# Performance work log

Measured on AMD Instinct MI355X. Metric: run time of the kernel, lower is better.

The kernel has to match this reference:

```python
import jax, jax.numpy as jnp
import numpy as np

NUM_HEADS = 16


def setup_inputs() -> dict:
    key = jax.random.key(0)
    k1, k2, k3 = jax.random.split(key, 3)
    x = jax.random.normal(k1, (2, 2048, 1024), dtype=jnp.float32)
    w_qkv = jax.random.normal(k2, (3072, 1024), dtype=jnp.float32) * 0.02
    b_qkv = jax.random.normal(k3, (3072,), dtype=jnp.float32) * 0.02
    return {"x": x, "w_qkv": w_qkv, "b_qkv": b_qkv}


def reference(x, w_qkv, b_qkv):
    b, s, _ = x.shape
    d_model = w_qkv.shape[0] // 3
    head_dim = d_model // NUM_HEADS
    # fused QKV projection (torch Linear: x @ W^T + b)
    qkv = x @ w_qkv.T + b_qkv                      # [b, s, 3*d_model]
    qkv = qkv.reshape(b, s, NUM_HEADS, 3 * head_dim)
    qkv = jnp.transpose(qkv, (0, 2, 1, 3))          # [b, h, s, 3*hd]
    q, k, v = jnp.split(qkv, 3, axis=-1)            # each [b, h, s, hd]
    scale = 1.0 / np.sqrt(head_dim).astype(np.float32)
    scores = jnp.einsum("bhqd,bhkd->bhqk", q, k) * scale
    attn = jax.nn.softmax(scores, axis=-1)
    values = jnp.einsum("bhqk,bhkd->bhqd", attn, v)  # [b, h, s, hd]
    # Faithful to source: reshape WITHOUT permuting heads back (head-interleaved)
    return values.reshape(b, s, d_model)
```

## Files before the change

kernel.cpp:

```cpp
#include <hip/hip_runtime.h>
#include <cstdint>

typedef unsigned short ushort_t;

#define M_ROWS 4096
#define N_COLS 3072
#define K_DIM  1024
#define S_LEN  2048
#define NHEADS 16
#define HDIM   64
#define QSCALE 0.1803368801111204f

typedef __bf16 bf16_t;
typedef bf16_t  bf16x8  __attribute__((ext_vector_type(8)));
typedef short   shortx4 __attribute__((ext_vector_type(4)));
typedef float   floatx4 __attribute__((ext_vector_type(4)));
typedef ushort_t ushortx4 __attribute__((ext_vector_type(4)));

union U32x2S4 { unsigned u[2]; shortx4 s; };

__device__ __forceinline__ unsigned short f2bf(float f) {
  unsigned u = __float_as_uint(f);
  u += 0x7FFFu + ((u >> 16) & 1u);
  return (unsigned short)(u >> 16);
}

__device__ __forceinline__ unsigned pkbf(float a, float b) {
  unsigned ua = __float_as_uint(a) + 0x8000u;
  unsigned ub = __float_as_uint(b) + 0x8000u;
  return __builtin_amdgcn_perm(ub, ua, 0x07060302u);
}

__device__ __forceinline__ unsigned cvtpk(float a, float b) {
#if __has_builtin(__builtin_amdgcn_cvt_pk_bf16_f32)
  auto t = __builtin_amdgcn_cvt_pk_bf16_f32(a, b);
  unsigned r;
  __builtin_memcpy(&r, &t, 4);
  return r;
#else
  return pkbf(a, b);
#endif
}

__device__ __forceinline__ float fexp2(float x) {
#if __has_builtin(__builtin_amdgcn_exp2f)
  return __builtin_amdgcn_exp2f(x);
#else
  float r; asm volatile("v_exp_f32 %0, %1\n\ts_nop 1" : "=v"(r) : "v"(x)); return r;
#endif
}

__device__ __forceinline__ void gload_lds16(const void* g, void* l) {
  __builtin_amdgcn_global_load_lds(
      (const __attribute__((address_space(1))) unsigned int*)g,
      (__attribute__((address_space(3))) unsigned int*)l,
      16, 0, 0);
}

__global__ __launch_bounds__(256) void cvt_bf16_kernel(
    const float* __restrict__ x, const float* __restrict__ w,
    ushort_t* __restrict__ Xb, ushort_t* __restrict__ Wb) {
  const int NX8 = (M_ROWS * K_DIM) / 8;
  int i = blockIdx.x * 256 + threadIdx.x;
  const float4* src;
  ushort_t* dst;
  int idx;
  if (i < NX8) { src = (const float4*)x; dst = Xb; idx = i; }
  else         { src = (const float4*)w; dst = Wb; idx = i - NX8; }
  float4 a = src[2 * idx];
  float4 b = src[2 * idx + 1];
  uint4 o;
  o.x = cvtpk(a.x, a.y);
  o.y = cvtpk(a.z, a.w);
  o.z = cvtpk(b.x, b.y);
  o.w = cvtpk(b.z, b.w);
  *(uint4*)(dst + 8 * (size_t)idx) = o;
}

__global__ __launch_bounds__(256) void qkv_gemm_kernel(
    const ushort_t* __restrict__ Xb, const ushort_t* __restrict__ Wb,
    const float* __restrict__ bias,
    ushort_t* __restrict__ Qb, ushort_t* __restrict__ Kb, ushort_t* __restrict__ Vb) {
  __shared__ ushort_t As[128 * 64];
  __shared__ ushort_t Bs[128 * 64];
  const int tid = threadIdx.x;
  const int l = tid & 63, w = tid >> 6;
  const int quad = l >> 4, lj = l & 15;
  const int m0 = blockIdx.y * 128, n0 = blockIdx.x * 128;
  const int wm = (w & 1) * 64, wn = (w >> 1) * 64;

  floatx4 acc[4][4] = {};

  const int srow = w * 32 + (l >> 3);
  const int scol = ((l & 7) ^ (l >> 3)) * 8;
  const ushort_t* gA = Xb + (size_t)(m0 + srow) * K_DIM + scol;
  const ushort_t* gB = Wb + (size_t)(n0 + srow) * K_DIM + scol;
  ushort_t* lA = As + (w * 32) * 64;
  ushort_t* lB = Bs + (w * 32) * 64;

  const int swr = lj & 7;

  for (int k0 = 0; k0 < K_DIM; k0 += 64) {
    __syncthreads();
#pragma unroll
    for (int c = 0; c < 4; ++c) {
      gload_lds16(gA + (size_t)(c * 8) * K_DIM + k0, lA + c * 8 * 64);
      gload_lds16(gB + (size_t)(c * 8) * K_DIM + k0, lB + c * 8 * 64);
    }
    __syncthreads();
#pragma unroll
    for (int kk = 0; kk < 2; ++kk) {
      const int ch = ((kk * 4 + quad) ^ swr) * 8;
      bf16x8 aF[4], bF[4];
#pragma unroll
      for (int i = 0; i < 4; ++i)
        aF[i] = *(const bf16x8*)(As + (wm + i * 16 + lj) * 64 + ch);
#pragma unroll
      for (int j = 0; j < 4; ++j)
        bF[j] = *(const bf16x8*)(Bs + (wn + j * 16 + lj) * 64 + ch);
#pragma unroll
      for (int i = 0; i < 4; ++i)
#pragma unroll
        for (int j = 0; j < 4; ++j)
          acc[i][j] = __builtin_amdgcn_mfma_f32_16x16x32_bf16(aF[i], bF[j], acc[i][j], 0, 0, 0);
    }
  }

#pragma unroll
  for (int j = 0; j < 4; ++j) {
    const int n = n0 + wn + j * 16 + lj;
    const int h = n / 192;
    const int r = n - h * 192;
    const int seg = r >> 6;
    const int d = r & 63;
    const float bv = bias[n];
    ushort_t* dst = (seg == 0) ? Qb : (seg == 1) ? Kb : Vb;
    const float scl = (seg == 0) ? QSCALE : 1.0f;
    const size_t base = (size_t)h * S_LEN * HDIM + d;
#pragma unroll
    for (int i = 0; i < 4; ++i) {
#pragma unroll
      for (int rg = 0; rg < 4; ++rg) {
        const int m = m0 + wm + i * 16 + quad * 4 + rg;
        const int bi = m >> 11;
        const int si = m & 2047;
        dst[base + ((size_t)bi * NHEADS * S_LEN + si) * HDIM] =
            f2bf((acc[i][j][rg] + bv) * scl);
      }
    }
  }
}

__global__ __launch_bounds__(512, 4) void attn_kernel(
    const ushort_t* __restrict__ Qb, const ushort_t* __restrict__ Kb,
    const ushort_t* __restrict__ Vb, float* __restrict__ out) {
  __shared__ ushort_t Ks[2][128 * 64];
  __shared__ ushort_t Vs[2][64 * 140];
  const int tid = threadIdx.x;
  const int l = tid & 63, w = tid >> 6;
  const int quad = l >> 4, lj = l & 15;
  const int id = (blockIdx.x & 7) * 64 + (blockIdx.x >> 3);
  const int bh = id >> 4;
  const int qt = id & 15;
  const int q0 = qt * 128 + w * 16;
  const size_t headoff = (size_t)bh * S_LEN * HDIM;

  bf16x8 qF[2];
#pragma unroll
  for (int kk = 0; kk < 2; ++kk)
    qF[kk] = *(const bf16x8*)(Qb + headoff + (size_t)(q0 + lj) * HDIM +
                              kk * 32 + quad * 8);

  floatx4 accO[4] = {};
  float l_runA = 0.f, l_runB = 0.f;

  const int kr = tid >> 3;
  const int kc = ((tid & 7) ^ (kr & 7)) * 8;
  const ushort_t* gK = Kb + headoff + (size_t)kr * HDIM + kc;

  const int dq = tid & 15;
  const int spw = tid >> 4;
  const ushort_t* gV = Vb + headoff + dq * 4;
  const int swz = (dq >> 2) << 1;

  const int swk = lj & 7;

  {
    uint2 va[2], vb[2];
#pragma unroll
    for (int R = 0; R < 2; ++R) {
      const ushort_t* g = gV + (size_t)(2 * (R * 32 + spw)) * HDIM;
      va[R] = *(const uint2*)g;
      vb[R] = *(const uint2*)(g + HDIM);
    }
#pragma unroll
    for (int c = 0; c < 2; ++c)
      gload_lds16(gK + (size_t)(c * 64) * HDIM, &Ks[0][0] + tid * 8 + c * 64 * 64);
    unsigned* vdst = (unsigned*)&Vs[0][0];
#pragma unroll
    for (int R = 0; R < 2; ++R) {
      const int sp = R * 32 + spw;
      unsigned o0 = __builtin_amdgcn_perm(vb[R].x, va[R].x, 0x05040100u);
      unsigned o1 = __builtin_amdgcn_perm(vb[R].x, va[R].x, 0x07060302u);
      unsigned o2 = __builtin_amdgcn_perm(vb[R].y, va[R].y, 0x05040100u);
      unsigned o3 = __builtin_amdgcn_perm(vb[R].y, va[R].y, 0x07060302u);
      const int sp2 = sp ^ swz;
      vdst[(4 * dq + 0) * 70 + sp2] = o0;
      vdst[(4 * dq + 1) * 70 + sp2] = o1;
      vdst[(4 * dq + 2) * 70 + sp2] = o2;
      vdst[(4 * dq + 3) * 70 + sp2] = o3;
    }
  }
  __syncthreads();

  for (int kb = 0; kb < 16; ++kb) {
    const int cur = kb & 1;
    const ushort_t* Kc = &Ks[cur][0];
    const ushort_t* Vc = &Vs[cur][0];

    uint2 va[2], vb[2];
    if (kb < 15) {
      const int kv1 = (kb + 1) * 128;
#pragma unroll
      for (int R = 0; R < 2; ++R) {
        const ushort_t* g = gV + (size_t)(kv1 + 2 * (R * 32 + spw)) * HDIM;
        va[R] = *(const uint2*)g;
        vb[R] = *(const uint2*)(g + HDIM);
      }
#pragma unroll
      for (int c = 0; c < 2; ++c)
        gload_lds16(gK + (size_t)(kv1 + c * 64) * HDIM,
                    &Ks[cur ^ 1][0] + tid * 8 + c * 64 * 64);
    }

    floatx4 accST[8];
#pragma unroll
    for (int c = 0; c < 8; ++c) {
      const ushort_t* krow = Kc + (c * 16 + lj) * 64;
      bf16x8 kF0 = *(const bf16x8*)(krow + ((quad ^ swk) * 8));
      bf16x8 kF1 = *(const bf16x8*)(krow + (((quad ^ swk) ^ 4) * 8));
      floatx4 z = {0.f, 0.f, 0.f, 0.f};
      z = __builtin_amdgcn_mfma_f32_16x16x32_bf16(kF0, qF[0], z, 0, 0, 0);
      accST[c] = __builtin_amdgcn_mfma_f32_16x16x32_bf16(kF1, qF[1], z, 0, 0, 0);
    }

    shortx4 aP[8];
    float lsA = 0.f, lsB = 0.f;
#pragma unroll
    for (int c = 0; c < 8; ++c) {
      float p0 = fexp2(accST[c][0]);
      float p1 = fexp2(accST[c][1]);
      float p2 = fexp2(accST[c][2]);
      float p3 = fexp2(accST[c][3]);
      lsA += p0 + p1;
      lsB += p2 + p3;
      U32x2S4 t;
      t.u[0] = cvtpk(p0, p1);
      t.u[1] = cvtpk(p2, p3);
      aP[c] = t.s;
    }
    l_runA += lsA;
    l_runB += lsB;

    if (kb < 15) {
      unsigned* vdst = (unsigned*)&Vs[cur ^ 1][0];
#pragma unroll
      for (int R = 0; R < 2; ++R) {
        const int sp = R * 32 + spw;
        unsigned o0 = __builtin_amdgcn_perm(vb[R].x, va[R].x, 0x05040100u);
        unsigned o1 = __builtin_amdgcn_perm(vb[R].x, va[R].x, 0x07060302u);
        unsigned o2 = __builtin_amdgcn_perm(vb[R].y, va[R].y, 0x05040100u);
        unsigned o3 = __builtin_amdgcn_perm(vb[R].y, va[R].y, 0x07060302u);
        const int sp2 = sp ^ swz;
        vdst[(4 * dq + 0) * 70 + sp2] = o0;
        vdst[(4 * dq + 1) * 70 + sp2] = o1;
        vdst[(4 * dq + 2) * 70 + sp2] = o2;
        vdst[(4 * dq + 3) * 70 + sp2] = o3;
      }
    }

#pragma unroll
    for (int dt = 0; dt < 4; ++dt) {
      const ushort_t* vp = Vc + (dt * 16 + lj) * 140 + (quad ^ dt) * 4;
#pragma unroll
      for (int c = 0; c < 8; ++c) {
        shortx4 vF = *(const shortx4*)(vp + c * 16);
        accO[dt] = __builtin_amdgcn_mfma_f32_16x16x16bf16_1k(aP[c], vF, accO[dt], 0, 0, 0);
      }
    }

    __syncthreads();
  }

  {
    float ls = l_runA + l_runB;
    ls += __shfl_xor(ls, 16, 64);
    ls += __shfl_xor(ls, 32, 64);
    const float inv = 1.0f / ls;
    const int sbase = (l & 48) | (quad * 4);
    float iv[4];
    iv[0] = __shfl(inv, sbase + 0, 64);
    iv[1] = __shfl(inv, sbase + 1, 64);
    iv[2] = __shfl(inv, sbase + 2, 64);
    iv[3] = __shfl(inv, sbase + 3, 64);
#pragma unroll
    for (int dt = 0; dt < 4; ++dt) {
#pragma unroll
      for (int rg = 0; rg < 4; ++rg) {
        const int q = q0 + quad * 4 + rg;
        out[headoff + (size_t)q * HDIM + dt * 16 + lj] = accO[dt][rg] * iv[rg];
      }
    }
  }
}

extern "C" void kernel_launch(void* const* d_in, const int* in_sizes, int n_in,
                              void* d_out, int out_size, void* d_ws, size_t ws_size,
                              hipStream_t stream) {
  (void)in_sizes; (void)n_in; (void)out_size; (void)ws_size;
  const float* x  = (const float*)d_in[0];
  const float* wq = (const float*)d_in[1];
  const float* bq = (const float*)d_in[2];
  float* out = (float*)d_out;

  char* ws = (char*)d_ws;
  ushort_t* Qb = (ushort_t*)(ws);
  ushort_t* Kb = (ushort_t*)(ws + 8388608);
  ushort_t* Vb = (ushort_t*)(ws + 16777216);
  ushort_t* Xb = (ushort_t*)(ws + 25165824);
  ushort_t* Wb = (ushort_t*)(ws + 33554432);

  cvt_bf16_kernel<<<3584, 256, 0, stream>>>(x, wq, Xb, Wb);
  qkv_gemm_kernel<<<dim3(N_COLS / 128, M_ROWS / 128), 256, 0, stream>>>(Xb, Wb, bq, Qb, Kb, Vb);
  attn_kernel<<<512, 512, 0, stream>>>(Qb, Kb, Vb, out);
}
```

Before: 162.8 us.

## Process 32 query rows per wave to reuse K/V LDS fragments

Each attention wave now handles two 16-row query tiles instead of one, so a block covers 256 queries and the grid shrinks from 512 to 256 blocks. Every K and V fragment read from shared memory feeds two MFMAs, which halves LDS traffic and global K/V loads per query. In exchange, register pressure rises (the launch-bounds occupancy hint drops from 4 to 2) and there are only 256 blocks, which may underfill the GPU's compute units.

```diff
diff --git a/kernel.cpp b/kernel.cpp
--- a/kernel.cpp
+++ b/kernel.cpp
@@ -151,7 +151,7 @@
   }
 }
 
-__global__ __launch_bounds__(512, 4) void attn_kernel(
+__global__ __launch_bounds__(512, 2) void attn_kernel(
     const ushort_t* __restrict__ Qb, const ushort_t* __restrict__ Kb,
     const ushort_t* __restrict__ Vb, float* __restrict__ out) {
   __shared__ ushort_t Ks[2][128 * 64];
@@ -159,20 +159,23 @@
   const int tid = threadIdx.x;
   const int l = tid & 63, w = tid >> 6;
   const int quad = l >> 4, lj = l & 15;
-  const int id = (blockIdx.x & 7) * 64 + (blockIdx.x >> 3);
-  const int bh = id >> 4;
-  const int qt = id & 15;
-  const int q0 = qt * 128 + w * 16;
+  const int id = (blockIdx.x & 7) * 32 + (blockIdx.x >> 3);
+  const int bh = id >> 3;
+  const int qt = id & 7;
+  const int q0 = qt * 256 + w * 32;
   const size_t headoff = (size_t)bh * S_LEN * HDIM;
 
-  bf16x8 qF[2];
-#pragma unroll
-  for (int kk = 0; kk < 2; ++kk)
-    qF[kk] = *(const bf16x8*)(Qb + headoff + (size_t)(q0 + lj) * HDIM +
-                              kk * 32 + quad * 8);
-
-  floatx4 accO[4] = {};
-  float l_runA = 0.f, l_runB = 0.f;
+  bf16x8 qF[2][2];
+#pragma unroll
+  for (int qh = 0; qh < 2; ++qh)
+#pragma unroll
+    for (int kk = 0; kk < 2; ++kk)
+      qF[qh][kk] = *(const bf16x8*)(Qb + headoff +
+                                    (size_t)(q0 + qh * 16 + lj) * HDIM +
+                                    kk * 32 + quad * 8);
+
+  floatx4 accO[2][4] = {};
+  float l_runA[2] = {0.f, 0.f}, l_runB[2] = {0.f, 0.f};
 
   const int kr = tid >> 3;
   const int kc = ((tid & 7) ^ (kr & 7)) * 8;
@@ -233,34 +236,41 @@
                     &Ks[cur ^ 1][0] + tid * 8 + c * 64 * 64);
     }
 
-    floatx4 accST[8];
+    floatx4 accST[2][8];
 #pragma unroll
     for (int c = 0; c < 8; ++c) {
       const ushort_t* krow = Kc + (c * 16 + lj) * 64;
       bf16x8 kF0 = *(const bf16x8*)(krow + ((quad ^ swk) * 8));
       bf16x8 kF1 = *(const bf16x8*)(krow + (((quad ^ swk) ^ 4) * 8));
-      floatx4 z = {0.f, 0.f, 0.f, 0.f};
-      z = __builtin_amdgcn_mfma_f32_16x16x32_bf16(kF0, qF[0], z, 0, 0, 0);
-      accST[c] = __builtin_amdgcn_mfma_f32_16x16x32_bf16(kF1, qF[1], z, 0, 0, 0);
-    }
-
-    shortx4 aP[8];
-    float lsA = 0.f, lsB = 0.f;
-#pragma unroll
-    for (int c = 0; c < 8; ++c) {
-      float p0 = fexp2(accST[c][0]);
-      float p1 = fexp2(accST[c][1]);
-      float p2 = fexp2(accST[c][2]);
-      float p3 = fexp2(accST[c][3]);
-      lsA += p0 + p1;
-      lsB += p2 + p3;
-      U32x2S4 t;
-      t.u[0] = cvtpk(p0, p1);
-      t.u[1] = cvtpk(p2, p3);
-      aP[c] = t.s;
-    }
-    l_runA += lsA;
-    l_runB += lsB;
+#pragma unroll
+      for (int qh = 0; qh < 2; ++qh) {
+        floatx4 z = {0.f, 0.f, 0.f, 0.f};
+        z = __builtin_amdgcn_mfma_f32_16x16x32_bf16(kF0, qF[qh][0], z, 0, 0, 0);
+        accST[qh][c] =
+            __builtin_amdgcn_mfma_f32_16x16x32_bf16(kF1, qF[qh][1], z, 0, 0, 0);
+      }
+    }
+
+    shortx4 aP[2][8];
+#pragma unroll
+    for (int qh = 0; qh < 2; ++qh) {
+      float lsA = 0.f, lsB = 0.f;
+#pragma unroll
+      for (int c = 0; c < 8; ++c) {
+        float p0 = fexp2(accST[qh][c][0]);
+        float p1 = fexp2(accST[qh][c][1]);
+        float p2 = fexp2(accST[qh][c][2]);
+        float p3 = fexp2(accST[qh][c][3]);
+        lsA += p0 + p1;
+        lsB += p2 + p3;
+        U32x2S4 t;
+        t.u[0] = cvtpk(p0, p1);
+        t.u[1] = cvtpk(p2, p3);
+        aP[qh][c] = t.s;
+      }
+      l_runA[qh] += lsA;
+      l_runB[qh] += lsB;
+    }
 
     if (kb < 15) {
       unsigned* vdst = (unsigned*)&Vs[cur ^ 1][0];
@@ -285,15 +295,19 @@
 #pragma unroll
       for (int c = 0; c < 8; ++c) {
         shortx4 vF = *(const shortx4*)(vp + c * 16);
-        accO[dt] = __builtin_amdgcn_mfma_f32_16x16x16bf16_1k(aP[c], vF, accO[dt], 0, 0, 0);
+        accO[0][dt] =
+            __builtin_amdgcn_mfma_f32_16x16x16bf16_1k(aP[0][c], vF, accO[0][dt], 0, 0, 0);
+        accO[1][dt] =
+            __builtin_amdgcn_mfma_f32_16x16x16bf16_1k(aP[1][c], vF, accO[1][dt], 0, 0, 0);
       }
     }
 
     __syncthreads();
   }
 
-  {
-    float ls = l_runA + l_runB;
+#pragma unroll
+  for (int qh = 0; qh < 2; ++qh) {
+    float ls = l_runA[qh] + l_runB[qh];
     ls += __shfl_xor(ls, 16, 64);
     ls += __shfl_xor(ls, 32, 64);
     const float inv = 1.0f / ls;
@@ -307,8 +321,8 @@
     for (int dt = 0; dt < 4; ++dt) {
 #pragma unroll
       for (int rg = 0; rg < 4; ++rg) {
-        const int q = q0 + quad * 4 + rg;
-        out[headoff + (size_t)q * HDIM + dt * 16 + lj] = accO[dt][rg] * iv[rg];
+        const int q = q0 + qh * 16 + quad * 4 + rg;
+        out[headoff + (size_t)q * HDIM + dt * 16 + lj] = accO[qh][dt][rg] * iv[rg];
       }
     }
   }
@@ -332,5 +346,5 @@
 
   cvt_bf16_kernel<<<3584, 256, 0, stream>>>(x, wq, Xb, Wb);
   qkv_gemm_kernel<<<dim3(N_COLS / 128, M_ROWS / 128), 256, 0, stream>>>(Xb, Wb, bq, Qb, Kb, Vb);
-  attn_kernel<<<512, 512, 0, stream>>>(Qb, Kb, Vb, out);
-}
+  attn_kernel<<<256, 512, 0, stream>>>(Qb, Kb, Vb, out);
+}
```

New measurement: 160.4 us. Within noise of the previous version (-1.4%).
